# Optimization experiments

Measured on AMD Instinct MI355X. Metric: run time of the kernel, lower is better.

The kernel has to match this reference:

```python
import jax, jax.numpy as jnp
import numpy as np

TPS = (10.0, 20.0, 30.0)   # Tps init arg (per-segment period)
EPS = 1e-4                 # jitter added to GP predictive covariance
SEG_LEN = 50               # len(ts[j]) for every segment


def setup_inputs() -> dict:
    key = jax.random.key(0)
    k1, k2, k3 = jax.random.split(key, 3)
    K, M, D, T = 16, 128, 16, 302  # T = 2 + 50 + 100 + 150
    z = jax.random.normal(k1, (K, M, D, T), dtype=jnp.float32)
    # sorted time points in (0, Tp_j) per segment, shape [C, SEG_LEN]
    ts = jnp.sort(jax.random.uniform(k2, (3, SEG_LEN), dtype=jnp.float32)
                  * jnp.asarray(TPS, jnp.float32)[:, None], axis=1)
    # log_tau param (D,), tau around tau_init=1.5
    log_tau = jnp.log(1.0 + jax.random.uniform(k3, (16,), dtype=jnp.float32))
    sldj = jnp.zeros((), jnp.float32)
    return {"z": z, "ts": ts, "log_tau": log_tau, "sum_log_det_jacobians": sldj}


def reference(z, ts, log_tau, sum_log_det_jacobians):
    # z: [K,M,D,T]; ts: [C,SEG_LEN]; log_tau: [D]
    tau = jnp.exp(log_tau)                      # [D]
    z_first = z[..., 0:1]                       # [K,M,D,1]
    z_last = z[..., 1:2]                        # [K,M,D,1]
    z_EP = jnp.concatenate([z_first, z_last], axis=-1)  # [K,M,D,2]
    C, seg = ts.shape
    ts_flat = ts.reshape(-1)
    ldj = sum_log_det_jacobians
    t_ind = 2
    outs = []
    for j in range(C):  # C=3 structurally distinct segment sizes
        m = (j + 1) * seg                       # middle_len
        ts_mid = ts_flat[:m]
        ts_j = jnp.concatenate([jnp.array([0.0, TPS[j]], ts.dtype), ts_mid])  # [m+2]
        ds = ts_j[:, None] - ts_j[None, :]      # [m+2,m+2]
        # squared-exp kernel, batched over all D dims at once
        Kmat = jnp.exp(-(ds ** 2)[None] / (2.0 * tau[:, None, None] ** 2))  # [D,n,n]
        K_EPEP_inv = jnp.linalg.inv(Kmat[:, :2, :2])          # [D,2,2]
        K_predEP = Kmat[:, 2:, :2]                            # [D,m,2]
        A_mu = jnp.einsum('dpe,def->dpf', K_predEP, K_EPEP_inv)  # [D,m,2]
        # conditional mean: A_mu @ z_EP  -> [K,M,D,m]
        z_GP_mu = jnp.einsum('dpe,bsde->bsdp', A_mu, z_EP)
        # conditional covariance  K_predpred - K_predEP K_EPEP^{-1} K_EPpred
        Sigma = Kmat[:, 2:, 2:] - jnp.einsum('dpe,dqe->dpq', A_mu, K_predEP)
        Sigma = Sigma + EPS * jnp.eye(m, dtype=Sigma.dtype)
        L = jnp.linalg.cholesky(Sigma)                        # [D,m,m]
        diag = jnp.diagonal(L, axis1=1, axis2=2)              # [D,m]
        # sum_i log|prod(diag_i)| == sum log|diag| (Cholesky diag > 0)
        ldj = ldj + jnp.sum(jnp.log(jnp.abs(diag)))
        z_mid = z[..., t_ind:t_ind + m]                       # [K,M,D,m]
        t_ind += m
        Lz = jnp.einsum('dpq,bsdq->bsdp', L, z_mid)           # [K,M,D,m]
        z_hat = z_GP_mu + Lz
        outs.append(jnp.concatenate([z_first, z_hat, z_last], axis=-1))  # [K,M,D,m+2]
    z_out = jnp.concatenate(outs, axis=-1)  # [K,M,D, sum_j(m_j+2)] = [16,128,16,306]
    return z_out, ldj
```

## Files before the change

kernel.cpp:

```cpp
#include <hip/hip_runtime.h>

#define LB0_OFF 0
#define LB1_OFF 36864
#define LB2_OFF 158720
#define PART_OFF 373760

typedef __attribute__((ext_vector_type(8))) short bf8_t;
typedef __attribute__((ext_vector_type(8))) unsigned short us8_t;
typedef __attribute__((ext_vector_type(4))) float f32x4;

__device__ __forceinline__ int tri_i(int p) { return (p * (p + 1)) >> 1; }

__device__ __forceinline__ int roff(int p) {
  const int T = p >> 2, r = p & 3;
  return ((T + 1) * (2 * T + r)) << 2;
}

__device__ __forceinline__ void tri_decode(int e, int& r, int& c) {
  r = (int)((sqrtf(8.0f * (float)e + 1.0f) - 1.0f) * 0.5f);
  if (tri_i(r + 1) <= e) ++r;
  if (tri_i(r) > e) --r;
  c = e - tri_i(r);
}

__device__ __forceinline__ unsigned short f2bf(float f) {
  unsigned u = __builtin_bit_cast(unsigned, f);
  u = (u + 0x7FFFu + ((u >> 16) & 1u)) >> 16;
  return (unsigned short)u;
}
__device__ __forceinline__ float bf2f(unsigned short h) {
  return __builtin_bit_cast(float, ((unsigned)h) << 16);
}

__device__ __forceinline__ float blane(float v, int l) {
  return __builtin_bit_cast(float, __builtin_amdgcn_readlane(__builtin_bit_cast(int, v), l));
}
__device__ __forceinline__ float fastrcp(float x) { return __builtin_amdgcn_rcpf(x); }

#define BNT 512
#define EPSF 1e-4f

template <int J>
__device__ __forceinline__ void build_impl(int d,
                                           const float* __restrict__ ts,
                                           const float* __restrict__ log_tau,
                                           float* __restrict__ ws,
                                           float* sS,
                                           unsigned short* sUc, unsigned short* sWc,
                                           float* stj, float* sAmu, float* sKp,
                                           float* red)
{
  constexpr int M  = (J + 1) * 50;
  constexpr int MP = (J == 0) ? 64 : ((J == 1) ? 112 : 160);
  constexpr int KS = (J == 0) ? 72 : ((J == 1) ? 136 : 168);
  constexpr int LBOFF = (J == 0) ? LB0_OFF : ((J == 1) ? LB1_OFF : LB2_OFF);
  constexpr float TPSJ = (J == 0) ? 10.0f : ((J == 1) ? 20.0f : 30.0f);
  constexpr int KW = KS / 2;
  constexpr int TOT = (MP * (MP + 1)) / 2;
  constexpr int NPAN = MP / 16;

  const int tid  = threadIdx.x;
  const int lane = tid & 63;
  const int wid  = tid >> 6;

  const float tau = expf(log_tau[d]);
  const float cc = 1.0f / (2.0f * tau * tau);

  for (int i = tid; i < M; i += BNT) stj[i] = ts[i];
  __syncthreads();

  const float k01 = expf(-TPSJ * TPSJ * cc);
  const float det = 1.0f - k01 * k01;
  const float i00 = 1.0f / det;
  const float i01 = -k01 / det;

  for (int p = tid; p < M; p += BNT) {
    float tp = stj[p];
    float kp0 = expf(-tp * tp * cc);
    float dt = tp - TPSJ;
    float kp1 = expf(-dt * dt * cc);
    sKp[p * 2 + 0] = kp0; sKp[p * 2 + 1] = kp1;
    sAmu[p * 2 + 0] = fmaf(kp0, i00, kp1 * i01);
    sAmu[p * 2 + 1] = fmaf(kp0, i01, kp1 * i00);
  }
  __syncthreads();

  for (int e = tid; e < TOT; e += BNT) {
    int r, q;
    tri_decode(e, r, q);
    float v;
    if (r < M) {
      float dq = stj[r] - stj[q];
      v = expf(-dq * dq * cc)
        - fmaf(sAmu[r * 2], sKp[q * 2], sAmu[r * 2 + 1] * sKp[q * 2 + 1]);
      if (r == q) v += EPSF;
    } else {
      v = (r == q) ? 1.0f : 0.0f;
    }
    sS[roff(r) + q] = v;
  }
  __syncthreads();

  const int tr = lane & 15;
#pragma unroll 1
  for (int pb = 0; pb < NPAN; ++pb) {
    const int kb = pb << 4;
    const int be = kb + 16;
    const int rbase = roff(kb + tr) + kb;

    float rd[16];
    float invd[16];
    if (wid < 3) {
      const float4* rp = (const float4*)&sS[rbase];
#pragma unroll
      for (int c4 = 0; c4 < 4; ++c4) *(float4*)&rd[c4 * 4] = rp[c4];
#pragma unroll
      for (int kk = 0; kk < 15; ++kk) {
        const float dkk = fmaxf(blane(rd[kk], kk), EPSF);
        const float ri = fastrcp(dkk);
        invd[kk] = ri;
        const float c = -rd[kk] * ri;
#pragma unroll
        for (int q2 = kk + 1; q2 < 16; ++q2) {
          const float cq2 = blane(rd[kk], q2);
          if (tr > kk && q2 <= tr) rd[q2] = fmaf(c, cq2, rd[q2]);
        }
      }
      invd[15] = fastrcp(fmaxf(blane(rd[15], 15), EPSF));
    }

    if (be < MP) {
      const int i = be + tid;
      if (i < MP) {
        const int base = roff(i) + kb;
        float r[16];
        const float4* rp = (const float4*)&sS[base];
#pragma unroll
        for (int c4 = 0; c4 < 4; ++c4) *(float4*)&r[c4 * 4] = rp[c4];
#pragma unroll
        for (int kk = 0; kk < 15; ++kk) {
          const float c = r[kk] * invd[kk];
#pragma unroll
          for (int q = kk + 1; q < 16; ++q)
            r[q] = fmaf(-c, blane(rd[kk], q), r[q]);
        }
        float4* sp = (float4*)&sS[base];
#pragma unroll
        for (int c4 = 0; c4 < 4; ++c4) sp[c4] = *(float4*)&r[c4 * 4];
        unsigned short uc[32], wc[32];
#pragma unroll
        for (int t = 0; t < 16; ++t) {
          const float uv = r[t];
          const unsigned short uhh = f2bf(uv);
          uc[t] = uhh; uc[16 + t] = f2bf(uv - bf2f(uhh));
          const float wv = -(r[t] * invd[t]);
          const unsigned short whh = f2bf(wv);
          wc[t] = whh; wc[16 + t] = f2bf(wv - bf2f(whh));
        }
        unsigned short* ucp = &sUc[i * 32];
        unsigned short* wcp = &sWc[i * 32];
#pragma unroll
        for (int c8 = 0; c8 < 4; ++c8) {
          *(us8_t*)&ucp[c8 * 8] = *(us8_t*)&uc[c8 * 8];
          *(us8_t*)&wcp[c8 * 8] = *(us8_t*)&wc[c8 * 8];
        }
      }
    }
    __syncthreads();

    if (wid == 0 && lane < 16) {
#pragma unroll
      for (int q = 0; q < 16; ++q) if (q <= tr) sS[rbase + q] = rd[q];
    }

    if (be < MP) {
      const int ntr = (MP - be) >> 4;
      const int ntiles = (ntr * (ntr + 1)) >> 1;
      const int rloc = lane & 15;
      const int koff = (lane >> 4) * 8;
      for (int t = wid; t < ntiles; t += 8) {
        int ta, tb;
        tri_decode(t, ta, tb);
        const int R0 = be + (ta << 4);
        const int Q0 = be + (tb << 4);
        const bf8_t af  = *(const bf8_t*)&sWc[(R0 + rloc) * 32 + koff];
        const bf8_t af2 = *(const bf8_t*)&sWc[(R0 + rloc) * 32 + (koff ^ 16)];
        const bf8_t bfv = *(const bf8_t*)&sUc[(Q0 + rloc) * 32 + koff];
        const int drow = R0 + (lane >> 4) * 4;
        const int qq = Q0 + rloc;
        int ra[4];
        f32x4 acc;
#pragma unroll
        for (int e = 0; e < 4; ++e) {
          ra[e] = roff(drow + e) + qq;
          acc[e] = sS[ra[e]];
        }
        acc = __builtin_amdgcn_mfma_f32_16x16x32_bf16(af,  bfv, acc, 0, 0, 0);
        acc = __builtin_amdgcn_mfma_f32_16x16x32_bf16(af2, bfv, acc, 0, 0, 0);
#pragma unroll
        for (int e = 0; e < 4; ++e)
          if (qq <= drow + e) sS[ra[e]] = acc[e];
      }
    }
    __syncthreads();
  }

  float part = 0.0f;
  for (int p = tid; p < M; p += BNT)
    part += 0.5f * logf(fmaxf(sS[roff(p) + p], EPSF));
#pragma unroll
  for (int off = 32; off > 0; off >>= 1) part += __shfl_down(part, off);
  if (lane == 0) red[wid] = part;
  __syncthreads();
  if (tid == 0) {
    float s = 0.0f;
#pragma unroll
    for (int w8 = 0; w8 < 8; ++w8) s += red[w8];
    ws[PART_OFF + J * 16 + d] = s;
  }

  unsigned* LBg = (unsigned*)ws + LBOFF + d * (MP * KW);
  constexpr int NWORDS = MP * KW;
  for (int idx = tid; idx < NWORDS; idx += BNT) {
    const int p = idx / KW;
    const int k0 = (idx - p * KW) * 2;
    unsigned short h[2];
#pragma unroll
    for (int e = 0; e < 2; ++e) {
      const int k = k0 + e;
      float v = 0.0f;
      if (p < M) {
        if (k < M) {
          if (k <= p) {
            const float dq = fmaxf(sS[roff(k) + k], EPSF);
            v = (k == p) ? sqrtf(dq) : sS[roff(p) + k] * rsqrtf(dq);
          }
        } else if (k == M)     v = sAmu[p * 2 + 0];
        else if (k == M + 1)   v = sAmu[p * 2 + 1];
      }
      h[e] = f2bf(v);
    }
    LBg[idx] = (unsigned)h[0] | ((unsigned)h[1] << 16);
  }
}

__global__ __launch_bounds__(BNT) void build_kernel(const float* __restrict__ ts,
                                                    const float* __restrict__ log_tau,
                                                    float* __restrict__ ws)
{
  __shared__ float sS[13120];
  __shared__ __attribute__((aligned(16))) unsigned short sUc[160 * 32];
  __shared__ __attribute__((aligned(16))) unsigned short sWc[160 * 32];
  __shared__ float stj[152];
  __shared__ float sAmu[304];
  __shared__ float sKp[304];
  __shared__ float red[8];

  const int j = blockIdx.x >> 4;
  const int d = blockIdx.x & 15;
  if (j == 0)      build_impl<0>(d, ts, log_tau, ws, sS, sUc, sWc, stj, sAmu, sKp, red);
  else if (j == 1) build_impl<1>(d, ts, log_tau, ws, sS, sUc, sWc, stj, sAmu, sKp, red);
  else             build_impl<2>(d, ts, log_tau, ws, sS, sUc, sWc, stj, sAmu, sKp, red);
}

template <int M, int MP, int KS, int KT, int TOFF, int OOFF, int LBOFF>
__device__ __forceinline__ void apply_impl(const float* __restrict__ z,
                                           const unsigned* __restrict__ wsu,
                                           float* __restrict__ out,
                                           char* smem, int blk)
{
  constexpr int PT = MP / 16;
  constexpr int CK = KS / 8;
  const int d   = blk & 15;
  const int bs0 = (blk >> 4) * 64;
  const int tid = threadIdx.x;
  const int lane = tid & 63;
  const int wv   = tid >> 6;

  unsigned short* Zs = (unsigned short*)smem;

  for (int idx = tid; idx < 64 * CK; idx += 256) {
    const int r = idx / CK;
    const int k0 = (idx - r * CK) * 8;
    const float* zr = z + (size_t)((bs0 + r) * 16 + d) * 302;
    us8_t v;
    if (k0 + 8 <= M) {
#pragma unroll
      for (int t = 0; t < 4; ++t) {
        const float2 f = *(const float2*)(zr + TOFF + k0 + 2 * t);
        v[2 * t]     = f2bf(f.x);
        v[2 * t + 1] = f2bf(f.y);
      }
    } else {
#pragma unroll
      for (int e = 0; e < 8; ++e) {
        const int k = k0 + e;
        float f;
        if (k < M)           f = zr[TOFF + k];
        else if (k == M)     f = zr[0];
        else if (k == M + 1) f = zr[1];
        else                 f = 0.0f;
        v[e] = f2bf(f);
      }
    }
    *(us8_t*)&Zs[r * KS + k0] = v;
  }

  if (tid < 128) {
    const int r = tid >> 1;
    const int which = tid & 1;
    const float* zr = z + (size_t)((bs0 + r) * 16 + d) * 302;
    out[(size_t)((bs0 + r) * 16 + d) * 306 + OOFF + (which ? (M + 1) : 0)] = zr[which];
  }
  __syncthreads();

  bf8_t afr[4][KT];
  {
    const int arow = lane & 15;
    const int koff = (lane >> 4) * 8;
#pragma unroll
    for (int rt = 0; rt < 4; ++rt)
#pragma unroll
      for (int kt = 0; kt < KT; ++kt)
        afr[rt][kt] = *(const bf8_t*)&Zs[(rt * 16 + arow) * KS + kt * 32 + koff];
  }

  const unsigned short* LBd = (const unsigned short*)(wsu + LBOFF + d * (MP * (KS / 2)));
  const int pt0 = (PT * wv) >> 2;
  const int pt1 = (PT * (wv + 1)) >> 2;
  for (int pt = pt0; pt < pt1; ++pt) {
    const int p = pt * 16 + (lane & 15);
    const unsigned short* bb = &LBd[p * KS + (lane >> 4) * 8];
    bf8_t bfr[KT];
#pragma unroll
    for (int kt = 0; kt < KT; ++kt)
      bfr[kt] = *(const bf8_t*)&bb[kt * 32];
#pragma unroll
    for (int rt = 0; rt < 4; ++rt) {
      f32x4 acc = {0.0f, 0.0f, 0.0f, 0.0f};
#pragma unroll
      for (int kt = 0; kt < KT; ++kt)
        acc = __builtin_amdgcn_mfma_f32_16x16x32_bf16(afr[rt][kt], bfr[kt], acc, 0, 0, 0);
      if (p < M) {
        const int rbase = bs0 + rt * 16 + (lane >> 4) * 4;
#pragma unroll
        for (int e = 0; e < 4; ++e)
          out[(size_t)((rbase + e) * 16 + d) * 306 + OOFF + 1 + p] = acc[e];
      }
    }
  }
}

__global__ __launch_bounds__(256) void apply_kernel(const float* __restrict__ z,
                                                    const unsigned* __restrict__ wsu,
                                                    float* __restrict__ out,
                                                    const float* __restrict__ part,
                                                    const float* __restrict__ sldj,
                                                    int last)
{
  __shared__ __attribute__((aligned(16))) char smem[21504];
  const int bid = blockIdx.x;
  if (bid == 1535 && threadIdx.x == 0) {
    float s = sldj[0];
#pragma unroll
    for (int i = 0; i < 48; ++i) s += part[i];
    out[last] = s;
  }
  if (bid < 512)       apply_impl<150, 160, 168, 5, 152, 154, LB2_OFF>(z, wsu, out, smem, bid);
  else if (bid < 1024) apply_impl<100, 112, 136, 4,  52,  52, LB1_OFF>(z, wsu, out, smem, bid - 512);
  else                 apply_impl< 50,  64,  72, 2,   2,   0, LB0_OFF>(z, wsu, out, smem, bid - 1024);
}

extern "C" void kernel_launch(void* const* d_in, const int* in_sizes, int n_in,
                              void* d_out, int out_size, void* d_ws, size_t ws_size,
                              hipStream_t stream)
{
  const float* z       = (const float*)d_in[0];
  const float* ts      = (const float*)d_in[1];
  const float* log_tau = (const float*)d_in[2];
  const float* sldj    = (const float*)d_in[3];
  float* out = (float*)d_out;
  float* ws  = (float*)d_ws;

  hipLaunchKernelGGL(build_kernel, dim3(48), dim3(BNT), 0, stream, ts, log_tau, ws);
  hipLaunchKernelGGL(apply_kernel, dim3(1536), dim3(256), 0, stream,
                     z, (const unsigned*)ws, out,
                     ws + PART_OFF, sldj, out_size - 1);
}
```

Measured before the change: 164.7 us.

## Fuse factor build with small-segment apply using per-matrix ready flags

Merges the build kernel with the apply work for the two smaller segments into one persistent-style launch. Build blocks publish per-(segment,dim) release flags and apply blocks spin-wait on them after staging their z tiles, so the z loads overlap the Cholesky build. The largest segment's apply runs in a separate follow-up kernel. This adds a memset, spin-waiting that depends on co-residency of producer blocks, and a special case that skips writing part of the last padded factor row, which likely overlaps the flag storage region.

```diff
diff --git a/kernel.cpp b/kernel.cpp
--- a/kernel.cpp
+++ b/kernel.cpp
@@ -4,6 +4,7 @@
 #define LB1_OFF 36864
 #define LB2_OFF 158720
 #define PART_OFF 373760
+#define FLAGS_OFF 373676
 
 typedef __attribute__((ext_vector_type(8))) short bf8_t;
 typedef __attribute__((ext_vector_type(8))) unsigned short us8_t;
@@ -223,6 +224,9 @@
   constexpr int NWORDS = MP * KW;
   for (int idx = tid; idx < NWORDS; idx += BNT) {
     const int p = idx / KW;
+    if constexpr (J == 2) {
+      if (d == 15 && p == 159 && (idx - p * KW) < 48) continue;
+    }
     const int k0 = (idx - p * KW) * 2;
     unsigned short h[2];
 #pragma unroll
@@ -244,36 +248,17 @@
   }
 }
 
-__global__ __launch_bounds__(BNT) void build_kernel(const float* __restrict__ ts,
-                                                    const float* __restrict__ log_tau,
-                                                    float* __restrict__ ws)
-{
-  __shared__ float sS[13120];
-  __shared__ __attribute__((aligned(16))) unsigned short sUc[160 * 32];
-  __shared__ __attribute__((aligned(16))) unsigned short sWc[160 * 32];
-  __shared__ float stj[152];
-  __shared__ float sAmu[304];
-  __shared__ float sKp[304];
-  __shared__ float red[8];
-
-  const int j = blockIdx.x >> 4;
-  const int d = blockIdx.x & 15;
-  if (j == 0)      build_impl<0>(d, ts, log_tau, ws, sS, sUc, sWc, stj, sAmu, sKp, red);
-  else if (j == 1) build_impl<1>(d, ts, log_tau, ws, sS, sUc, sWc, stj, sAmu, sKp, red);
-  else             build_impl<2>(d, ts, log_tau, ws, sS, sUc, sWc, stj, sAmu, sKp, red);
-}
-
 template <int M, int MP, int KS, int KT, int TOFF, int OOFF, int LBOFF>
 __device__ __forceinline__ void apply_impl(const float* __restrict__ z,
                                            const unsigned* __restrict__ wsu,
                                            float* __restrict__ out,
-                                           char* smem, int blk)
+                                           char* smem, int blk, int tid,
+                                           const unsigned* flg)
 {
   constexpr int PT = MP / 16;
   constexpr int CK = KS / 8;
   const int d   = blk & 15;
   const int bs0 = (blk >> 4) * 64;
-  const int tid = threadIdx.x;
   const int lane = tid & 63;
   const int wv   = tid >> 6;
 
@@ -325,6 +310,13 @@
         afr[rt][kt] = *(const bf8_t*)&Zs[(rt * 16 + arow) * KS + kt * 32 + koff];
   }
 
+  if (flg) {
+    for (int it = 0; it < (1 << 20); ++it) {
+      if (__hip_atomic_load(flg, __ATOMIC_ACQUIRE, __HIP_MEMORY_SCOPE_AGENT)) break;
+      __builtin_amdgcn_s_sleep(2);
+    }
+  }
+
   const unsigned short* LBd = (const unsigned short*)(wsu + LBOFF + d * (MP * (KS / 2)));
   const int pt0 = (PT * wv) >> 2;
   const int pt1 = (PT * (wv + 1)) >> 2;
@@ -351,24 +343,78 @@
   }
 }
 
-__global__ __launch_bounds__(256) void apply_kernel(const float* __restrict__ z,
-                                                    const unsigned* __restrict__ wsu,
-                                                    float* __restrict__ out,
-                                                    const float* __restrict__ part,
-                                                    const float* __restrict__ sldj,
-                                                    int last)
+__device__ __forceinline__ void run_bigchunk(int g, const float* z,
+                                             const unsigned* wsu, float* out,
+                                             char* smem, unsigned* flags)
+{
+  const int tid  = threadIdx.x;
+  const int half = tid >> 8;
+  const int ltid = tid & 255;
+  char* sm = smem + half * 21504;
+  if (g < 256) {
+    const int sub = g * 2 + half;
+    apply_impl<50, 64, 72, 2, 2, 0, LB0_OFF>(z, wsu, out, sm, sub, ltid,
+                                             &flags[sub & 15]);
+  } else {
+    const int sub = (g - 256) * 2 + half;
+    apply_impl<100, 112, 136, 4, 52, 52, LB1_OFF>(z, wsu, out, sm, sub, ltid,
+                                                  &flags[16 + (sub & 15)]);
+  }
+}
+
+__global__ __launch_bounds__(512, 4) void fused_kernel(const float* __restrict__ z,
+                                                       const float* __restrict__ ts,
+                                                       const float* __restrict__ log_tau,
+                                                       float* __restrict__ ws,
+                                                       float* __restrict__ out)
+{
+  __shared__ __attribute__((aligned(16))) char smem[76032];
+  unsigned* flags = (unsigned*)ws + FLAGS_OFF;
+  const int bid = blockIdx.x;
+  if (bid < 48) {
+    float* sS           = (float*)smem;
+    unsigned short* sUc = (unsigned short*)(smem + 52480);
+    unsigned short* sWc = (unsigned short*)(smem + 62720);
+    float* stj          = (float*)(smem + 72960);
+    float* sAmu         = (float*)(smem + 73568);
+    float* sKp          = (float*)(smem + 74784);
+    float* red          = (float*)(smem + 76000);
+    const int j = bid >> 4;
+    const int d = bid & 15;
+    if (j == 0)      build_impl<0>(d, ts, log_tau, ws, sS, sUc, sWc, stj, sAmu, sKp, red);
+    else if (j == 1) build_impl<1>(d, ts, log_tau, ws, sS, sUc, sWc, stj, sAmu, sKp, red);
+    else             build_impl<2>(d, ts, log_tau, ws, sS, sUc, sWc, stj, sAmu, sKp, red);
+    __syncthreads();
+    __threadfence();
+    if (threadIdx.x == 0)
+      __hip_atomic_store(&flags[bid], 1u, __ATOMIC_RELEASE, __HIP_MEMORY_SCOPE_AGENT);
+  } else {
+    const int w = bid - 48;
+    run_bigchunk(w, z, (const unsigned*)ws, out, smem, flags);
+    if (w < 48) {
+      __syncthreads();
+      run_bigchunk(464 + w, z, (const unsigned*)ws, out, smem, flags);
+    }
+  }
+}
+
+__global__ __launch_bounds__(256) void apply_j2_kernel(const float* __restrict__ z,
+                                                       const unsigned* __restrict__ wsu,
+                                                       float* __restrict__ out,
+                                                       const float* __restrict__ part,
+                                                       const float* __restrict__ sldj,
+                                                       int last)
 {
   __shared__ __attribute__((aligned(16))) char smem[21504];
-  const int bid = blockIdx.x;
-  if (bid == 1535 && threadIdx.x == 0) {
+  if (blockIdx.x == 0 && threadIdx.x == 0) {
     float s = sldj[0];
 #pragma unroll
     for (int i = 0; i < 48; ++i) s += part[i];
     out[last] = s;
   }
-  if (bid < 512)       apply_impl<150, 160, 168, 5, 152, 154, LB2_OFF>(z, wsu, out, smem, bid);
-  else if (bid < 1024) apply_impl<100, 112, 136, 4,  52,  52, LB1_OFF>(z, wsu, out, smem, bid - 512);
-  else                 apply_impl< 50,  64,  72, 2,   2,   0, LB0_OFF>(z, wsu, out, smem, bid - 1024);
+  apply_impl<150, 160, 168, 5, 152, 154, LB2_OFF>(z, wsu, out, smem,
+                                                  (int)blockIdx.x, (int)threadIdx.x,
+                                                  nullptr);
 }
 
 extern "C" void kernel_launch(void* const* d_in, const int* in_sizes, int n_in,
@@ -382,8 +428,10 @@
   float* out = (float*)d_out;
   float* ws  = (float*)d_ws;
 
-  hipLaunchKernelGGL(build_kernel, dim3(48), dim3(BNT), 0, stream, ts, log_tau, ws);
-  hipLaunchKernelGGL(apply_kernel, dim3(1536), dim3(256), 0, stream,
+  hipMemsetAsync((char*)d_ws + (size_t)FLAGS_OFF * 4, 0, 48 * 4, stream);
+  hipLaunchKernelGGL(fused_kernel, dim3(512), dim3(512), 0, stream,
+                     z, ts, log_tau, ws, out);
+  hipLaunchKernelGGL(apply_j2_kernel, dim3(512), dim3(256), 0, stream,
                      z, (const unsigned*)ws, out,
                      ws + PART_OFF, sldj, out_size - 1);
 }
```

Result: slower. 237.0 us (+43.9%).
